# Performance work log

Hardware: AMD Instinct MI355X
Metric: run time of the kernel (lower is better)

The kernel has to match this reference:

```python
import jax, jax.numpy as jnp
import numpy as np

N = 100000
E = 1600000
D_IN = 128
H = 128


def _param(key, shape, scale=0.05):
    return jax.random.normal(key, shape, dtype=jnp.float32) * scale


def setup_inputs() -> dict:
    key = jax.random.key(0)
    ks = jax.random.split(key, 24)
    inp = {
        'x': jax.random.normal(ks[0], (N, D_IN), dtype=jnp.float32),
        'edge_index': jax.random.randint(ks[1], (2, E), 0, N, dtype=jnp.int64),
        'h1': jax.random.normal(ks[2], (N, H), dtype=jnp.float32),
        'h2': jax.random.normal(ks[3], (N, H), dtype=jnp.float32),
        'h3': jax.random.normal(ks[4], (N, H), dtype=jnp.float32),
        # GCNConv params (PyG: lin weight applied as x @ W, W: [in, out] here)
        'gcn1_w': _param(ks[5], (D_IN, H)),
        'gcn1_b': jnp.zeros((H,), jnp.float32),
        'gcn2_w': _param(ks[6], (H, H)),
        'gcn2_b': jnp.zeros((H,), jnp.float32),
    }
    # torch.nn.GRUCell params: weight_ih [3H, in], weight_hh [3H, H], biases [3H]
    for i, kw in zip((1, 2, 3), (ks[7], ks[10], ks[13])):
        k1, k2, k3 = jax.random.split(kw, 3)
        inp[f'gru{i}_wih'] = _param(k1, (3 * H, H))
        inp[f'gru{i}_whh'] = _param(k2, (3 * H, H))
        inp[f'gru{i}_bih'] = _param(k3, (3 * H,))
        inp[f'gru{i}_bhh'] = jnp.zeros((3 * H,), jnp.float32)
    return inp


def gcn_conv(x, src, dst, w, b):
    """PyG GCNConv: D^-1/2 (A+I) D^-1/2 X W + b (symmetric norm, self-loops)."""
    xw = x @ w  # [N, H]
    ones = jnp.ones((src.shape[0],), xw.dtype)
    # degree including self-loop
    deg = jax.ops.segment_sum(ones, dst, num_segments=N) + 1.0
    dinv = jax.lax.rsqrt(deg)
    norm = dinv[src] * dinv[dst]  # [E]
    agg = jax.ops.segment_sum(xw[src] * norm[:, None], dst, num_segments=N)
    # self-loop contribution: norm = dinv[i]*dinv[i] = 1/deg[i]
    return agg + xw / deg[:, None] + b


def gru_cell(x, h, w_ih, w_hh, b_ih, b_hh):
    gi = x @ w_ih.T + b_ih  # [N, 3H]
    gh = h @ w_hh.T + b_hh
    i_r, i_z, i_n = jnp.split(gi, 3, axis=-1)
    h_r, h_z, h_n = jnp.split(gh, 3, axis=-1)
    r = jax.nn.sigmoid(i_r + h_r)
    z = jax.nn.sigmoid(i_z + h_z)
    n = jnp.tanh(i_n + r * h_n)
    return (1.0 - z) * n + z * h


def reference(x, edge_index, h1, h2, h3,
              gcn1_w, gcn1_b, gcn2_w, gcn2_b,
              gru1_wih, gru1_whh, gru1_bih, gru1_bhh,
              gru2_wih, gru2_whh, gru2_bih, gru2_bhh,
              gru3_wih, gru3_whh, gru3_bih, gru3_bhh):
    src, dst = edge_index[0], edge_index[1]
    x = jax.nn.relu(gcn_conv(x, src, dst, gcn1_w, gcn1_b))
    # dropout is identity at eval
    x = jax.nn.relu(gcn_conv(x, src, dst, gcn2_w, gcn2_b))
    h1n = gru_cell(x, h1, gru1_wih, gru1_whh, gru1_bih, gru1_bhh)
    h2n = gru_cell(h1n, h2, gru2_wih, gru2_whh, gru2_bih, gru2_bhh)
    h3n = gru_cell(h2n, h3, gru3_wih, gru3_whh, gru3_bih, gru3_bhh)
    return (h1n, h2n, h3n)
```

## Files before the change

### kernel.cpp

```cpp
#include <hip/hip_runtime.h>
#include <hip/hip_bf16.h>

#define DH 128
#define SCB 1024
#define NCHUNK 256
#define LROW 136

typedef __attribute__((ext_vector_type(8))) short short8_t;
typedef __attribute__((ext_vector_type(4))) float f32x4;
typedef __attribute__((ext_vector_type(2))) float f32x2;

static __device__ __forceinline__ short f2bf(float f) {
    union { float f; unsigned u; } v; v.f = f;
    unsigned r = v.u + 0x7fffu + ((v.u >> 16) & 1u);
    return (short)(r >> 16);
}

static __device__ __forceinline__ float bf2f(unsigned short b) {
    union { unsigned u; float f; } v; v.u = ((unsigned)b) << 16;
    return v.f;
}

static __device__ __forceinline__ short8_t cvt8(const float* p) {
    float4 a0 = *(const float4*)p;
    float4 a1 = *(const float4*)(p + 4);
    short8_t t;
    t[0] = f2bf(a0.x); t[1] = f2bf(a0.y); t[2] = f2bf(a0.z); t[3] = f2bf(a0.w);
    t[4] = f2bf(a1.x); t[5] = f2bf(a1.y); t[6] = f2bf(a1.z); t[7] = f2bf(a1.w);
    return t;
}

static __device__ __forceinline__ short8_t cvt8v(float4 a0, float4 a1) {
    short8_t t;
    t[0] = f2bf(a0.x); t[1] = f2bf(a0.y); t[2] = f2bf(a0.z); t[3] = f2bf(a0.w);
    t[4] = f2bf(a1.x); t[5] = f2bf(a1.y); t[6] = f2bf(a1.z); t[7] = f2bf(a1.w);
    return t;
}

static __device__ __forceinline__ float sigm(float x) {
    return __builtin_amdgcn_rcpf(1.f + __expf(-x));
}
static __device__ __forceinline__ float tanh_f(float x) {
    return 1.f - 2.f * __builtin_amdgcn_rcpf(__expf(2.f * x) + 1.f);
}

__global__ __launch_bounds__(256) void deg2_k(const int* __restrict__ ei, int E,
                                              unsigned* __restrict__ cnt, int span, int chunkE) {
    int r = blockIdx.x & 7;
    int c = blockIdx.x >> 3;
    int lo = r * span, hi = lo + span;
    long long e0 = (long long)c * chunkE;
    long long e1 = e0 + chunkE; if (e1 > E) e1 = E;
    for (long long e = e0 + threadIdx.x; e < e1; e += 256) {
        int d = ei[E + e];
        if (d >= lo && d < hi) atomicAdd(&cnt[d], 1u);
    }
}

__global__ __launch_bounds__(256) void scan1_k(const unsigned* __restrict__ cnt, int N,
                                               int* __restrict__ offs, unsigned* __restrict__ bsum) {
    __shared__ unsigned s[256];
    int t = threadIdx.x;
    int i0 = blockIdx.x * SCB + t * 4;
    unsigned v0 = (i0 + 0 < N) ? cnt[i0 + 0] : 0u;
    unsigned v1 = (i0 + 1 < N) ? cnt[i0 + 1] : 0u;
    unsigned v2 = (i0 + 2 < N) ? cnt[i0 + 2] : 0u;
    unsigned v3 = (i0 + 3 < N) ? cnt[i0 + 3] : 0u;
    unsigned ts = v0 + v1 + v2 + v3;
    s[t] = ts;
    __syncthreads();
    for (int off = 1; off < 256; off <<= 1) {
        unsigned u = (t >= off) ? s[t - off] : 0u;
        __syncthreads();
        s[t] += u;
        __syncthreads();
    }
    unsigned ex = s[t] - ts;
    if (i0 + 0 < N) offs[i0 + 0] = (int)ex;
    if (i0 + 1 < N) offs[i0 + 1] = (int)(ex + v0);
    if (i0 + 2 < N) offs[i0 + 2] = (int)(ex + v0 + v1);
    if (i0 + 3 < N) offs[i0 + 3] = (int)(ex + v0 + v1 + v2);
    if (t == 255) bsum[blockIdx.x] = s[255];
}

__global__ __launch_bounds__(1024) void scan2_k(unsigned* __restrict__ bsum, int B) {
    __shared__ unsigned s[1024];
    int t = threadIdx.x;
    unsigned v = (t < B) ? bsum[t] : 0u;
    s[t] = v;
    __syncthreads();
    for (int off = 1; off < 1024; off <<= 1) {
        unsigned u = (t >= off) ? s[t - off] : 0u;
        __syncthreads();
        s[t] += u;
        __syncthreads();
    }
    if (t < B) bsum[t] = s[t] - v;
    if (t == 0) bsum[B] = s[1023];
}

__global__ void scan3_k(int* __restrict__ offs, int* __restrict__ cur,
                        float* __restrict__ dinv, const unsigned* __restrict__ cnt,
                        const unsigned* __restrict__ bsum, int N, int B) {
    int i = blockIdx.x * 256 + threadIdx.x;
    if (i < N) {
        int v = offs[i] + (int)bsum[i >> 10];
        offs[i] = v;
        cur[i] = v;
        dinv[i] = rsqrtf((float)cnt[i] + 1.0f);
    }
    if (i == 0) offs[N] = (int)bsum[B];
}

__global__ __launch_bounds__(256) void fill2_k(const int* __restrict__ ei, int E,
                                               int* __restrict__ cur, int* __restrict__ csr_src,
                                               int span, int chunkE) {
    int r = blockIdx.x & 7;
    int c = blockIdx.x >> 3;
    int lo = r * span, hi = lo + span;
    long long e0 = (long long)c * chunkE;
    long long e1 = e0 + chunkE; if (e1 > E) e1 = E;
    for (long long e = e0 + threadIdx.x; e < e1; e += 256) {
        int d = ei[E + e];
        if (d >= lo && d < hi) {
            int pos = atomicAdd(&cur[d], 1);
            csr_src[pos] = ei[e];
        }
    }
}

__global__ void f2bf6_k(const float* __restrict__ s0, const float* __restrict__ s1,
                        const float* __restrict__ s2, const float* __restrict__ s3,
                        const float* __restrict__ s4, const float* __restrict__ s5,
                        short* __restrict__ dst, int WN) {
    int i = blockIdx.x * 256 + threadIdx.x;
    if (i >= 6 * WN) return;
    int b = i / WN, r = i - b * WN;
    const float* srcs[6] = {s0, s1, s2, s3, s4, s5};
    dst[i] = f2bf(srcs[b][r]);
}

__global__ void transpose_bf2_k(const float* __restrict__ sa, const float* __restrict__ sb,
                                short* __restrict__ da, short* __restrict__ db) {
    int i = blockIdx.x * 256 + threadIdx.x;
    int m = i >> 14;
    int j = i & 16383;
    int c = j >> 7, k = j & 127;
    const float* s = m ? sb : sa;
    short* d = m ? db : da;
    d[j] = f2bf(s[k * DH + c]);
}

__global__ __launch_bounds__(256, 4) void gemm_mfma_k(const float* __restrict__ A,
                                                      const short* __restrict__ Wt,
                                                      const float* __restrict__ dinv,
                                                      unsigned char* __restrict__ C, int N) {
    int tid = threadIdx.x;
    int wave = tid >> 6, lane = tid & 63;
    int lr = lane & 15, kg = lane >> 4;

    int row0 = blockIdx.x * 128 + wave * 32;
    int ar0 = min(row0 + lr, N - 1);
    int ar1 = min(row0 + 16 + lr, N - 1);
    const float* a0p = A + (size_t)ar0 * DH;
    const float* a1p = A + (size_t)ar1 * DH;
    short8_t af[2][4];
#pragma unroll
    for (int ks = 0; ks < 4; ks++) {
        af[0][ks] = cvt8(a0p + ks * 32 + kg * 8);
        af[1][ks] = cvt8(a1p + ks * 32 + kg * 8);
    }

    float di0[4], di1[4];
#pragma unroll
    for (int j = 0; j < 4; j++) {
        di0[j] = dinv[min(row0 + kg * 4 + j, N - 1)];
        di1[j] = dinv[min(row0 + 16 + kg * 4 + j, N - 1)];
    }

    short8_t bt[3][4];
#define GLOADW(slot, t) { \
    const short* wp = Wt + (size_t)((t) * 16 + lr) * DH + kg * 8; \
    bt[slot][0] = *(const short8_t*)(wp); \
    bt[slot][1] = *(const short8_t*)(wp + 32); \
    bt[slot][2] = *(const short8_t*)(wp + 64); \
    bt[slot][3] = *(const short8_t*)(wp + 96); }

    GLOADW(0, 0)
    GLOADW(1, 1)
#pragma unroll
    for (int t = 0; t < 8; t++) {
        if (t < 6) GLOADW((t + 2) % 3, t + 2)
        f32x4 acc0 = {0.f, 0.f, 0.f, 0.f};
        f32x4 acc1 = {0.f, 0.f, 0.f, 0.f};
#pragma unroll
        for (int ks = 0; ks < 4; ks++) {
            acc0 = __builtin_amdgcn_mfma_f32_16x16x32_bf16(af[0][ks], bt[t % 3][ks], acc0, 0, 0, 0);
            acc1 = __builtin_amdgcn_mfma_f32_16x16x32_bf16(af[1][ks], bt[t % 3][ks], acc1, 0, 0, 0);
        }
        int col = t * 16 + lr;
#pragma unroll
        for (int j = 0; j < 4; j++) {
            int g0 = row0 + kg * 4 + j;
            int g1 = row0 + 16 + kg * 4 + j;
            float v0 = acc0[j] * di0[j];
            float v1 = acc1[j] * di1[j];
            if (g0 < N) C[(size_t)g0 * DH + col] =
                (unsigned char)__builtin_amdgcn_cvt_pk_fp8_f32(v0, v0, 0u, false);
            if (g1 < N) C[(size_t)g1 * DH + col] =
                (unsigned char)__builtin_amdgcn_cvt_pk_fp8_f32(v1, v1, 0u, false);
        }
    }
#undef GLOADW
}

__global__ __launch_bounds__(256) void gather_k(const int* __restrict__ csr_src,
                                                const int* __restrict__ offs,
                                                const float* __restrict__ dinv,
                                                const unsigned short* __restrict__ xq2,
                                                const float* __restrict__ bias,
                                                float* __restrict__ dest, int N) {
    int wid = blockIdx.x * 4 + (threadIdx.x >> 6);
    if (wid >= N) return;
    int lane = threadIdx.x & 63;
    int j = offs[wid];
    int end = offs[wid + 1];
    float dd = dinv[wid];

    f32x2 f0 = __builtin_amdgcn_cvt_pk_f32_fp8((unsigned)xq2[(size_t)wid * 64 + lane], false);
    float ax = f0[0];
    float ay = f0[1];

#define ACC(w) { f32x2 f_ = __builtin_amdgcn_cvt_pk_f32_fp8((unsigned)(w), false); \
                 ax += f_[0]; ay += f_[1]; }

    if (j + 4 <= end) {
        int a0 = csr_src[j], a1 = csr_src[j + 1], a2 = csr_src[j + 2], a3 = csr_src[j + 3];
        j += 4;
        for (; j + 4 <= end; j += 4) {
            unsigned w0 = xq2[(size_t)a0 * 64 + lane];
            unsigned w1 = xq2[(size_t)a1 * 64 + lane];
            unsigned w2 = xq2[(size_t)a2 * 64 + lane];
            unsigned w3 = xq2[(size_t)a3 * 64 + lane];
            a0 = csr_src[j]; a1 = csr_src[j + 1]; a2 = csr_src[j + 2]; a3 = csr_src[j + 3];
            ACC(w0) ACC(w1) ACC(w2) ACC(w3)
        }
        unsigned w0 = xq2[(size_t)a0 * 64 + lane];
        unsigned w1 = xq2[(size_t)a1 * 64 + lane];
        unsigned w2 = xq2[(size_t)a2 * 64 + lane];
        unsigned w3 = xq2[(size_t)a3 * 64 + lane];
        ACC(w0) ACC(w1) ACC(w2) ACC(w3)
    }
    for (; j < end; ++j) {
        unsigned w = xq2[(size_t)csr_src[j] * 64 + lane];
        ACC(w)
    }
#undef ACC

    float2 b2 = ((const float2*)bias)[lane];
    float ox = fmaxf(fmaf(dd, ax, b2.x), 0.f);
    float oy = fmaxf(fmaf(dd, ay, b2.y), 0.f);
    float2 o; o.x = ox; o.y = oy;
    ((float2*)dest)[(size_t)wid * 64 + lane] = o;
}

__global__ __launch_bounds__(512, 1) void gru3_mfma_k(
        const float* __restrict__ X, const float* __restrict__ H1,
        const float* __restrict__ H2, const float* __restrict__ H3,
        const short* __restrict__ w1i, const short* __restrict__ w1h,
        const short* __restrict__ w2i, const short* __restrict__ w2h,
        const short* __restrict__ w3i, const short* __restrict__ w3h,
        const float* __restrict__ bi1, const float* __restrict__ bh1,
        const float* __restrict__ bi2, const float* __restrict__ bh2,
        const float* __restrict__ bi3, const float* __restrict__ bh3,
        float* __restrict__ o1, float* __restrict__ o2, float* __restrict__ o3,
        int N) {
    __shared__ short lds[2][64 * LROW];
    int tid = threadIdx.x;
    int row0 = blockIdx.x * 64;
    int wave = tid >> 6, lane = tid & 63;
    int lr = lane & 15, kg = lane >> 4;
    int c0 = wave * 16;

    const short* wihs[3] = {w1i, w2i, w3i};
    const short* whhs[3] = {w1h, w2h, w3h};
    const float* bihs[3] = {bi1, bi2, bi3};
    const float* bhhs[3] = {bh1, bh2, bh3};
    float* outs[3] = {o1, o2, o3};

    short8_t bw[3][4], bu[3][4];
#define WLOADALL(wih_, whh_) { \
    _Pragma("unroll") \
    for (int g = 0; g < 3; g++) { \
        const short* wi = (wih_) + (size_t)(g * DH + c0 + lr) * DH + kg * 8; \
        const short* wh = (whh_) + (size_t)(g * DH + c0 + lr) * DH + kg * 8; \
        _Pragma("unroll") \
        for (int ks = 0; ks < 4; ks++) { \
            bw[g][ks] = *(const short8_t*)(wi + ks * 32); \
            bu[g][ks] = *(const short8_t*)(wh + ks * 32); \
        } \
    } }

    WLOADALL(w1i, w1h)

    {
        int mat = tid >> 8;
        int r = (tid & 255) >> 2;
        int q = tid & 3;
        int grow = min(row0 + r, N - 1);
        const float* src = (mat ? H1 : X) + (size_t)grow * DH + q * 32;
        char* dst = (char*)&lds[mat][r * LROW] + q * 64;
#pragma unroll
        for (int j = 0; j < 4; j++) {
            short8_t v = cvt8(src + j * 8);
            *(short8_t*)(dst + j * 16) = v;
        }
    }
    __syncthreads();

    int gcol = c0 + lr;
    int colb = gcol * 2;
    int srow = tid >> 3;
    int sq = tid & 7;

#pragma unroll
    for (int cell = 0; cell < 3; cell++) {
        f32x4 aR[4], aZ[4], aI[4], aH[4];
#pragma unroll
        for (int rt = 0; rt < 4; rt++) {
            aR[rt] = (f32x4){0,0,0,0}; aZ[rt] = (f32x4){0,0,0,0};
            aI[rt] = (f32x4){0,0,0,0}; aH[rt] = (f32x4){0,0,0,0};
        }
#pragma unroll
        for (int rt = 0; rt < 4; rt++) {
            int r = rt * 16 + lr;
            const char* xrow = (const char*)&lds[0][r * LROW];
            const char* hrow = (const char*)&lds[1][r * LROW];
            short8_t xa[4], ha[4];
#pragma unroll
            for (int ks = 0; ks < 4; ks++) {
                int boff = ks * 64 + kg * 16;
                xa[ks] = *(const short8_t*)(xrow + boff);
                ha[ks] = *(const short8_t*)(hrow + boff);
            }
#pragma unroll
            for (int ks = 0; ks < 4; ks++) {
                aR[rt] = __builtin_amdgcn_mfma_f32_16x16x32_bf16(xa[ks], bw[0][ks], aR[rt], 0, 0, 0);
                aR[rt] = __builtin_amdgcn_mfma_f32_16x16x32_bf16(ha[ks], bu[0][ks], aR[rt], 0, 0, 0);
                aZ[rt] = __builtin_amdgcn_mfma_f32_16x16x32_bf16(xa[ks], bw[1][ks], aZ[rt], 0, 0, 0);
                aZ[rt] = __builtin_amdgcn_mfma_f32_16x16x32_bf16(ha[ks], bu[1][ks], aZ[rt], 0, 0, 0);
                aI[rt] = __builtin_amdgcn_mfma_f32_16x16x32_bf16(xa[ks], bw[2][ks], aI[rt], 0, 0, 0);
                aH[rt] = __builtin_amdgcn_mfma_f32_16x16x32_bf16(ha[ks], bu[2][ks], aH[rt], 0, 0, 0);
            }
        }

        float4 hs0, hs1, hs2, hs3;
        if (cell < 2) {
            int grow = min(row0 + srow, N - 1);
            const float* src = (cell == 0 ? H2 : H3) + (size_t)grow * DH + sq * 16;
            hs0 = *(const float4*)(src + 0);
            hs1 = *(const float4*)(src + 4);
            hs2 = *(const float4*)(src + 8);
            hs3 = *(const float4*)(src + 12);
        }

        const float* bih = bihs[cell];
        const float* bhh = bhhs[cell];
        float br = bih[gcol], bz = bih[DH + gcol], bn = bih[2 * DH + gcol];
        float cr = bhh[gcol], cz = bhh[DH + gcol], cn = bhh[2 * DH + gcol];
        float* outp = outs[cell];
        short hb[4][4];
#pragma unroll
        for (int rt = 0; rt < 4; rt++) {
#pragma unroll
            for (int j = 0; j < 4; j++) {
                int r = rt * 16 + kg * 4 + j;
                float hv = bf2f(*(const unsigned short*)((const char*)&lds[1][r * LROW] + colb));
                float rr = sigm(aR[rt][j] + br + cr);
                float zz = sigm(aZ[rt][j] + bz + cz);
                float nn = tanh_f(aI[rt][j] + bn + rr * (aH[rt][j] + cn));
                float ov = (1.f - zz) * nn + zz * hv;
                int grow = row0 + r;
                if (grow < N) outp[(size_t)grow * DH + gcol] = ov;
                hb[rt][j] = f2bf(ov);
            }
        }

        if (cell < 2) {
            WLOADALL(wihs[cell + 1], whhs[cell + 1])
        }

        __syncthreads();

        if (cell < 2) {
#pragma unroll
            for (int rt = 0; rt < 4; rt++) {
#pragma unroll
                for (int j = 0; j < 4; j++) {
                    int r = rt * 16 + kg * 4 + j;
                    *(short*)((char*)&lds[0][r * LROW] + colb) = hb[rt][j];
                }
            }
            {
                char* dst = (char*)&lds[1][srow * LROW] + sq * 32;
                *(short8_t*)(dst) = cvt8v(hs0, hs1);
                *(short8_t*)(dst + 16) = cvt8v(hs2, hs3);
            }
            __syncthreads();
        }
    }
#undef WLOADALL
}

extern "C" void kernel_launch(void* const* d_in, const int* in_sizes, int n_in,
                              void* d_out, int out_size, void* d_ws, size_t ws_size,
                              hipStream_t stream) {
    const float* x    = (const float*)d_in[0];
    const int*   ei   = (const int*)d_in[1];
    const float* h1   = (const float*)d_in[2];
    const float* h2   = (const float*)d_in[3];
    const float* h3   = (const float*)d_in[4];
    const float* g1w  = (const float*)d_in[5];
    const float* g1b  = (const float*)d_in[6];
    const float* g2w  = (const float*)d_in[7];
    const float* g2b  = (const float*)d_in[8];
    const float* wih1 = (const float*)d_in[9];
    const float* whh1 = (const float*)d_in[10];
    const float* bih1 = (const float*)d_in[11];
    const float* bhh1 = (const float*)d_in[12];
    const float* wih2 = (const float*)d_in[13];
    const float* whh2 = (const float*)d_in[14];
    const float* bih2 = (const float*)d_in[15];
    const float* bhh2 = (const float*)d_in[16];
    const float* wih3 = (const float*)d_in[17];
    const float* whh3 = (const float*)d_in[18];
    const float* bih3 = (const float*)d_in[19];
    const float* bhh3 = (const float*)d_in[20];

    int N = in_sizes[0] / DH;
    int E = in_sizes[1] / 2;
    int B = (N + SCB - 1) / SCB;
    int nstripes = (N + 127) / 128;
    int nblk64 = (N + 63) / 64;
    int span = (N + 7) / 8;
    int chunkE = (E + NCHUNK - 1) / NCHUNK;

    char* wsp = (char*)d_ws;
    auto alloc = [&](size_t bytes) -> char* {
        char* p = wsp;
        wsp += (bytes + 63) & ~(size_t)63;
        return p;
    };
    unsigned* cnt = (unsigned*)alloc((size_t)N * 4);
    int* offs     = (int*)alloc(((size_t)N + 1) * 4);
    int* cur      = (int*)alloc((size_t)N * 4);
    float* dinv   = (float*)alloc((size_t)N * 4);
    unsigned* bsum= (unsigned*)alloc(((size_t)B + 1) * 4);
    int* csr_src  = (int*)alloc((size_t)E * 4);
    unsigned char* xq = (unsigned char*)alloc((size_t)N * DH);
    float* x2     = (float*)alloc((size_t)N * DH * 4);
    short* w1t    = (short*)alloc((size_t)DH * DH * 2);
    short* w2t    = (short*)alloc((size_t)DH * DH * 2);
    const int WN = 3 * DH * DH;
    short* wbAll  = (short*)alloc((size_t)6 * WN * 2);
    short* wb[6];
    for (int i = 0; i < 6; i++) wb[i] = wbAll + (size_t)i * WN;

    float* out  = (float*)d_out;
    float* h1n  = out;
    float* h2n  = out + (size_t)N * DH;
    float* h3n  = out + 2 * (size_t)N * DH;

    f2bf6_k<<<(6 * WN + 255) / 256, 256, 0, stream>>>(wih1, whh1, wih2, whh2, wih3, whh3, wbAll, WN);
    transpose_bf2_k<<<(2 * DH * DH + 255) / 256, 256, 0, stream>>>(g1w, g2w, w1t, w2t);

    hipMemsetAsync(cnt, 0, (size_t)N * 4, stream);
    deg2_k<<<8 * NCHUNK, 256, 0, stream>>>(ei, E, cnt, span, chunkE);
    scan1_k<<<B, 256, 0, stream>>>(cnt, N, offs, bsum);
    scan2_k<<<1, 1024, 0, stream>>>(bsum, B);
    scan3_k<<<(N + 255) / 256, 256, 0, stream>>>(offs, cur, dinv, cnt, bsum, N, B);
    fill2_k<<<8 * NCHUNK, 256, 0, stream>>>(ei, E, cur, csr_src, span, chunkE);

    int gblocks = (N + 3) / 4;

    gemm_mfma_k<<<nstripes, 256, 0, stream>>>(x, w1t, dinv, xq, N);
    gather_k<<<gblocks, 256, 0, stream>>>(csr_src, offs, dinv, (const unsigned short*)xq, g1b, x2, N);

    gemm_mfma_k<<<nstripes, 256, 0, stream>>>(x2, w2t, dinv, xq, N);
    gather_k<<<gblocks, 256, 0, stream>>>(csr_src, offs, dinv, (const unsigned short*)xq, g2b, x2, N);

    gru3_mfma_k<<<nblk64, 512, 0, stream>>>(x2, h1, h2, h3,
                                            wb[0], wb[1], wb[2], wb[3], wb[4], wb[5],
                                            bih1, bhh1, bih2, bhh2, bih3, bhh3,
                                            h1n, h2n, h3n, N);
}
```

Measured before the change: 531.0 us.

## Store intermediates in bf16 and make GRU kernel persistent with prefetch

The gather kernel now writes layer outputs as packed bf16 instead of fp32, and a new bf16-input GEMM consumes them directly, halving intermediate traffic. h1 is pre-converted to bf16 by a separate kernel. The GRU kernel becomes persistent over 512 blocks, with double-buffered LDS that prefetches the next stripe's X/H1 tiles during the last cell. The extra h1 conversion pass adds its own read and write of h1, and persistence may lower occupancy balance.

```diff
diff --git a/kernel.cpp b/kernel.cpp
--- a/kernel.cpp
+++ b/kernel.cpp
@@ -151,6 +151,14 @@
     d[j] = f2bf(s[k * DH + c]);
 }
 
+__global__ void h1bf_k(const float* __restrict__ src, unsigned* __restrict__ dst, long long n2) {
+    long long i = (long long)blockIdx.x * 256 + threadIdx.x;
+    if (i < n2) {
+        float2 v = ((const float2*)src)[i];
+        dst[i] = (unsigned)(unsigned short)f2bf(v.x) | ((unsigned)(unsigned short)f2bf(v.y) << 16);
+    }
+}
+
 __global__ __launch_bounds__(256, 4) void gemm_mfma_k(const float* __restrict__ A,
                                                       const short* __restrict__ Wt,
                                                       const float* __restrict__ dinv,
@@ -214,12 +222,75 @@
 #undef GLOADW
 }
 
+__global__ __launch_bounds__(256, 4) void gemm_mfma_bf_k(const short* __restrict__ A,
+                                                         const short* __restrict__ Wt,
+                                                         const float* __restrict__ dinv,
+                                                         unsigned char* __restrict__ C, int N) {
+    int tid = threadIdx.x;
+    int wave = tid >> 6, lane = tid & 63;
+    int lr = lane & 15, kg = lane >> 4;
+
+    int row0 = blockIdx.x * 128 + wave * 32;
+    int ar0 = min(row0 + lr, N - 1);
+    int ar1 = min(row0 + 16 + lr, N - 1);
+    const short* a0p = A + (size_t)ar0 * DH;
+    const short* a1p = A + (size_t)ar1 * DH;
+    short8_t af[2][4];
+#pragma unroll
+    for (int ks = 0; ks < 4; ks++) {
+        af[0][ks] = *(const short8_t*)(a0p + ks * 32 + kg * 8);
+        af[1][ks] = *(const short8_t*)(a1p + ks * 32 + kg * 8);
+    }
+
+    float di0[4], di1[4];
+#pragma unroll
+    for (int j = 0; j < 4; j++) {
+        di0[j] = dinv[min(row0 + kg * 4 + j, N - 1)];
+        di1[j] = dinv[min(row0 + 16 + kg * 4 + j, N - 1)];
+    }
+
+    short8_t bt[3][4];
+#define GLOADW(slot, t) { \
+    const short* wp = Wt + (size_t)((t) * 16 + lr) * DH + kg * 8; \
+    bt[slot][0] = *(const short8_t*)(wp); \
+    bt[slot][1] = *(const short8_t*)(wp + 32); \
+    bt[slot][2] = *(const short8_t*)(wp + 64); \
+    bt[slot][3] = *(const short8_t*)(wp + 96); }
+
+    GLOADW(0, 0)
+    GLOADW(1, 1)
+#pragma unroll
+    for (int t = 0; t < 8; t++) {
+        if (t < 6) GLOADW((t + 2) % 3, t + 2)
+        f32x4 acc0 = {0.f, 0.f, 0.f, 0.f};
+        f32x4 acc1 = {0.f, 0.f, 0.f, 0.f};
+#pragma unroll
+        for (int ks = 0; ks < 4; ks++) {
+            acc0 = __builtin_amdgcn_mfma_f32_16x16x32_bf16(af[0][ks], bt[t % 3][ks], acc0, 0, 0, 0);
+            acc1 = __builtin_amdgcn_mfma_f32_16x16x32_bf16(af[1][ks], bt[t % 3][ks], acc1, 0, 0, 0);
+        }
+        int col = t * 16 + lr;
+#pragma unroll
+        for (int j = 0; j < 4; j++) {
+            int g0 = row0 + kg * 4 + j;
+            int g1 = row0 + 16 + kg * 4 + j;
+            float v0 = acc0[j] * di0[j];
+            float v1 = acc1[j] * di1[j];
+            if (g0 < N) C[(size_t)g0 * DH + col] =
+                (unsigned char)__builtin_amdgcn_cvt_pk_fp8_f32(v0, v0, 0u, false);
+            if (g1 < N) C[(size_t)g1 * DH + col] =
+                (unsigned char)__builtin_amdgcn_cvt_pk_fp8_f32(v1, v1, 0u, false);
+        }
+    }
+#undef GLOADW
+}
+
 __global__ __launch_bounds__(256) void gather_k(const int* __restrict__ csr_src,
                                                 const int* __restrict__ offs,
                                                 const float* __restrict__ dinv,
                                                 const unsigned short* __restrict__ xq2,
                                                 const float* __restrict__ bias,
-                                                float* __restrict__ dest, int N) {
+                                                unsigned* __restrict__ dest, int N) {
     int wid = blockIdx.x * 4 + (threadIdx.x >> 6);
     if (wid >= N) return;
     int lane = threadIdx.x & 63;
@@ -260,12 +331,13 @@
     float2 b2 = ((const float2*)bias)[lane];
     float ox = fmaxf(fmaf(dd, ax, b2.x), 0.f);
     float oy = fmaxf(fmaf(dd, ay, b2.y), 0.f);
-    float2 o; o.x = ox; o.y = oy;
-    ((float2*)dest)[(size_t)wid * 64 + lane] = o;
-}
-
-__global__ __launch_bounds__(512, 1) void gru3_mfma_k(
-        const float* __restrict__ X, const float* __restrict__ H1,
+    unsigned o = (unsigned)(unsigned short)f2bf(ox) | ((unsigned)(unsigned short)f2bf(oy) << 16);
+    dest[(size_t)wid * 64 + lane] = o;
+}
+
+__global__ __launch_bounds__(512, 1) void gru3p_mfma_k(
+        const unsigned* __restrict__ Xb,
+        const unsigned* __restrict__ H1b,
         const float* __restrict__ H2, const float* __restrict__ H3,
         const short* __restrict__ w1i, const short* __restrict__ w1h,
         const short* __restrict__ w2i, const short* __restrict__ w2h,
@@ -274,10 +346,9 @@
         const float* __restrict__ bi2, const float* __restrict__ bh2,
         const float* __restrict__ bi3, const float* __restrict__ bh3,
         float* __restrict__ o1, float* __restrict__ o2, float* __restrict__ o3,
-        int N) {
-    __shared__ short lds[2][64 * LROW];
+        int N, int nstripes) {
+    __shared__ short lds[2][2][64 * LROW];
     int tid = threadIdx.x;
-    int row0 = blockIdx.x * 64;
     int wave = tid >> 6, lane = tid & 63;
     int lr = lane & 15, kg = lane >> 4;
     int c0 = wave * 16;
@@ -303,111 +374,140 @@
 
     WLOADALL(w1i, w1h)
 
-    {
-        int mat = tid >> 8;
-        int r = (tid & 255) >> 2;
-        int q = tid & 3;
-        int grow = min(row0 + r, N - 1);
-        const float* src = (mat ? H1 : X) + (size_t)grow * DH + q * 32;
-        char* dst = (char*)&lds[mat][r * LROW] + q * 64;
-#pragma unroll
-        for (int j = 0; j < 4; j++) {
-            short8_t v = cvt8(src + j * 8);
-            *(short8_t*)(dst + j * 16) = v;
-        }
-    }
-    __syncthreads();
-
     int gcol = c0 + lr;
     int colb = gcol * 2;
     int srow = tid >> 3;
     int sq = tid & 7;
-
-#pragma unroll
-    for (int cell = 0; cell < 3; cell++) {
-        f32x4 aR[4], aZ[4], aI[4], aH[4];
-#pragma unroll
-        for (int rt = 0; rt < 4; rt++) {
-            aR[rt] = (f32x4){0,0,0,0}; aZ[rt] = (f32x4){0,0,0,0};
-            aI[rt] = (f32x4){0,0,0,0}; aH[rt] = (f32x4){0,0,0,0};
-        }
-#pragma unroll
-        for (int rt = 0; rt < 4; rt++) {
-            int r = rt * 16 + lr;
-            const char* xrow = (const char*)&lds[0][r * LROW];
-            const char* hrow = (const char*)&lds[1][r * LROW];
-            short8_t xa[4], ha[4];
-#pragma unroll
-            for (int ks = 0; ks < 4; ks++) {
-                int boff = ks * 64 + kg * 16;
-                xa[ks] = *(const short8_t*)(xrow + boff);
-                ha[ks] = *(const short8_t*)(hrow + boff);
+    int pmat = tid >> 8;
+    int prow = (tid & 255) >> 2;
+    int pq = tid & 3;
+
+    int s = blockIdx.x;
+    if (s >= nstripes) return;
+
+    {
+        int grow = min(s * 64 + prow, N - 1);
+        const uint4* src4 = (const uint4*)((pmat ? H1b : Xb) + (size_t)grow * 64 + pq * 16);
+        uint4 a = src4[0], b = src4[1], c = src4[2], d = src4[3];
+        char* dst = (char*)&lds[0][pmat][prow * LROW] + pq * 64;
+        *(uint4*)(dst + 0)  = a;
+        *(uint4*)(dst + 16) = b;
+        *(uint4*)(dst + 32) = c;
+        *(uint4*)(dst + 48) = d;
+    }
+    __syncthreads();
+
+    int cur = 0;
+    for (; s < nstripes; ) {
+        int row0 = s * 64;
+        int snext = s + gridDim.x;
+        bool hasnext = snext < nstripes;
+        short* ldsX = lds[cur][0];
+        short* ldsH = lds[cur][1];
+        short* nxtX = lds[cur ^ 1][0];
+        short* nxtH = lds[cur ^ 1][1];
+        uint4 px0, px1, px2, px3;
+
+#pragma unroll
+        for (int cell = 0; cell < 3; cell++) {
+            f32x4 aR[4], aZ[4], aI[4], aH[4];
+#pragma unroll
+            for (int rt = 0; rt < 4; rt++) {
+                aR[rt] = (f32x4){0,0,0,0}; aZ[rt] = (f32x4){0,0,0,0};
+                aI[rt] = (f32x4){0,0,0,0}; aH[rt] = (f32x4){0,0,0,0};
             }
 #pragma unroll
-            for (int ks = 0; ks < 4; ks++) {
-                aR[rt] = __builtin_amdgcn_mfma_f32_16x16x32_bf16(xa[ks], bw[0][ks], aR[rt], 0, 0, 0);
-                aR[rt] = __builtin_amdgcn_mfma_f32_16x16x32_bf16(ha[ks], bu[0][ks], aR[rt], 0, 0, 0);
-                aZ[rt] = __builtin_amdgcn_mfma_f32_16x16x32_bf16(xa[ks], bw[1][ks], aZ[rt], 0, 0, 0);
-                aZ[rt] = __builtin_amdgcn_mfma_f32_16x16x32_bf16(ha[ks], bu[1][ks], aZ[rt], 0, 0, 0);
-                aI[rt] = __builtin_amdgcn_mfma_f32_16x16x32_bf16(xa[ks], bw[2][ks], aI[rt], 0, 0, 0);
-                aH[rt] = __builtin_amdgcn_mfma_f32_16x16x32_bf16(ha[ks], bu[2][ks], aH[rt], 0, 0, 0);
+            for (int rt = 0; rt < 4; rt++) {
+                int r = rt * 16 + lr;
+                const char* xrow = (const char*)&ldsX[r * LROW];
+                const char* hrow = (const char*)&ldsH[r * LROW];
+                short8_t xa[4], ha[4];
+#pragma unroll
+                for (int ks = 0; ks < 4; ks++) {
+                    int boff = ks * 64 + kg * 16;
+                    xa[ks] = *(const short8_t*)(xrow + boff);
+                    ha[ks] = *(const short8_t*)(hrow + boff);
+                }
+#pragma unroll
+                for (int ks = 0; ks < 4; ks++) {
+                    aR[rt] = __builtin_amdgcn_mfma_f32_16x16x32_bf16(xa[ks], bw[0][ks], aR[rt], 0, 0, 0);
+                    aR[rt] = __builtin_amdgcn_mfma_f32_16x16x32_bf16(ha[ks], bu[0][ks], aR[rt], 0, 0, 0);
+                    aZ[rt] = __builtin_amdgcn_mfma_f32_16x16x32_bf16(xa[ks], bw[1][ks], aZ[rt], 0, 0, 0);
+                    aZ[rt] = __builtin_amdgcn_mfma_f32_16x16x32_bf16(ha[ks], bu[1][ks], aZ[rt], 0, 0, 0);
+                    aI[rt] = __builtin_amdgcn_mfma_f32_16x16x32_bf16(xa[ks], bw[2][ks], aI[rt], 0, 0, 0);
+                    aH[rt] = __builtin_amdgcn_mfma_f32_16x16x32_bf16(ha[ks], bu[2][ks], aH[rt], 0, 0, 0);
+                }
             }
-        }
-
-        float4 hs0, hs1, hs2, hs3;
-        if (cell < 2) {
-            int grow = min(row0 + srow, N - 1);
-            const float* src = (cell == 0 ? H2 : H3) + (size_t)grow * DH + sq * 16;
-            hs0 = *(const float4*)(src + 0);
-            hs1 = *(const float4*)(src + 4);
-            hs2 = *(const float4*)(src + 8);
-            hs3 = *(const float4*)(src + 12);
-        }
-
-        const float* bih = bihs[cell];
-        const float* bhh = bhhs[cell];
-        float br = bih[gcol], bz = bih[DH + gcol], bn = bih[2 * DH + gcol];
-        float cr = bhh[gcol], cz = bhh[DH + gcol], cn = bhh[2 * DH + gcol];
-        float* outp = outs[cell];
-        short hb[4][4];
-#pragma unroll
-        for (int rt = 0; rt < 4; rt++) {
-#pragma unroll
-            for (int j = 0; j < 4; j++) {
-                int r = rt * 16 + kg * 4 + j;
-                float hv = bf2f(*(const unsigned short*)((const char*)&lds[1][r * LROW] + colb));
-                float rr = sigm(aR[rt][j] + br + cr);
-                float zz = sigm(aZ[rt][j] + bz + cz);
-                float nn = tanh_f(aI[rt][j] + bn + rr * (aH[rt][j] + cn));
-                float ov = (1.f - zz) * nn + zz * hv;
-                int grow = row0 + r;
-                if (grow < N) outp[(size_t)grow * DH + gcol] = ov;
-                hb[rt][j] = f2bf(ov);
+
+            float4 hs0, hs1, hs2, hs3;
+            if (cell < 2) {
+                int grow = min(row0 + srow, N - 1);
+                const float* src = (cell == 0 ? H2 : H3) + (size_t)grow * DH + sq * 16;
+                hs0 = *(const float4*)(src + 0);
+                hs1 = *(const float4*)(src + 4);
+                hs2 = *(const float4*)(src + 8);
+                hs3 = *(const float4*)(src + 12);
+            } else if (hasnext) {
+                int grow = min(snext * 64 + prow, N - 1);
+                const uint4* src4 = (const uint4*)((pmat ? H1b : Xb) + (size_t)grow * 64 + pq * 16);
+                px0 = src4[0]; px1 = src4[1]; px2 = src4[2]; px3 = src4[3];
             }
-        }
-
-        if (cell < 2) {
-            WLOADALL(wihs[cell + 1], whhs[cell + 1])
-        }
-
-        __syncthreads();
-
-        if (cell < 2) {
+
+            const float* bih = bihs[cell];
+            const float* bhh = bhhs[cell];
+            float br = bih[gcol], bz = bih[DH + gcol], bn = bih[2 * DH + gcol];
+            float cr = bhh[gcol], cz = bhh[DH + gcol], cn = bhh[2 * DH + gcol];
+            float* outp = outs[cell];
+            short hb[4][4];
 #pragma unroll
             for (int rt = 0; rt < 4; rt++) {
 #pragma unroll
                 for (int j = 0; j < 4; j++) {
                     int r = rt * 16 + kg * 4 + j;
-                    *(short*)((char*)&lds[0][r * LROW] + colb) = hb[rt][j];
+                    float hv = bf2f(*(const unsigned short*)((const char*)&ldsH[r * LROW] + colb));
+                    float rr = sigm(aR[rt][j] + br + cr);
+                    float zz = sigm(aZ[rt][j] + bz + cz);
+                    float nn = tanh_f(aI[rt][j] + bn + rr * (aH[rt][j] + cn));
+                    float ov = (1.f - zz) * nn + zz * hv;
+                    int grow = row0 + r;
+                    if (grow < N) outp[(size_t)grow * DH + gcol] = ov;
+                    hb[rt][j] = f2bf(ov);
                 }
             }
-            {
-                char* dst = (char*)&lds[1][srow * LROW] + sq * 32;
-                *(short8_t*)(dst) = cvt8v(hs0, hs1);
-                *(short8_t*)(dst + 16) = cvt8v(hs2, hs3);
+
+            if (cell < 2) {
+                WLOADALL(wihs[cell + 1], whhs[cell + 1])
+            } else if (hasnext) {
+                WLOADALL(w1i, w1h)
             }
-            __syncthreads();
-        }
+
+            if (cell < 2) {
+                __syncthreads();
+#pragma unroll
+                for (int rt = 0; rt < 4; rt++) {
+#pragma unroll
+                    for (int j = 0; j < 4; j++) {
+                        int r = rt * 16 + kg * 4 + j;
+                        *(short*)((char*)&ldsX[r * LROW] + colb) = hb[rt][j];
+                    }
+                }
+                {
+                    char* dst = (char*)&ldsH[srow * LROW] + sq * 32;
+                    *(short8_t*)(dst) = cvt8v(hs0, hs1);
+                    *(short8_t*)(dst + 16) = cvt8v(hs2, hs3);
+                }
+                __syncthreads();
+            } else if (hasnext) {
+                char* dst = (char*)&(pmat ? nxtH : nxtX)[prow * LROW] + pq * 64;
+                *(uint4*)(dst + 0)  = px0;
+                *(uint4*)(dst + 16) = px1;
+                *(uint4*)(dst + 32) = px2;
+                *(uint4*)(dst + 48) = px3;
+                __syncthreads();
+            }
+        }
+        cur ^= 1;
+        s = snext;
     }
 #undef WLOADALL
 }
@@ -458,7 +558,8 @@
     unsigned* bsum= (unsigned*)alloc(((size_t)B + 1) * 4);
     int* csr_src  = (int*)alloc((size_t)E * 4);
     unsigned char* xq = (unsigned char*)alloc((size_t)N * DH);
-    float* x2     = (float*)alloc((size_t)N * DH * 4);
+    unsigned* x2b = (unsigned*)alloc((size_t)N * DH * 2);
+    unsigned* h1b = (unsigned*)alloc((size_t)N * DH * 2);
     short* w1t    = (short*)alloc((size_t)DH * DH * 2);
     short* w2t    = (short*)alloc((size_t)DH * DH * 2);
     const int WN = 3 * DH * DH;
@@ -473,6 +574,8 @@
 
     f2bf6_k<<<(6 * WN + 255) / 256, 256, 0, stream>>>(wih1, whh1, wih2, whh2, wih3, whh3, wbAll, WN);
     transpose_bf2_k<<<(2 * DH * DH + 255) / 256, 256, 0, stream>>>(g1w, g2w, w1t, w2t);
+    long long n2 = (long long)N * DH / 2;
+    h1bf_k<<<(int)((n2 + 255) / 256), 256, 0, stream>>>(h1, h1b, n2);
 
     hipMemsetAsync(cnt, 0, (size_t)N * 4, stream);
     deg2_k<<<8 * NCHUNK, 256, 0, stream>>>(ei, E, cnt, span, chunkE);
@@ -484,13 +587,13 @@
     int gblocks = (N + 3) / 4;
 
     gemm_mfma_k<<<nstripes, 256, 0, stream>>>(x, w1t, dinv, xq, N);
-    gather_k<<<gblocks, 256, 0, stream>>>(csr_src, offs, dinv, (const unsigned short*)xq, g1b, x2, N);
-
-    gemm_mfma_k<<<nstripes, 256, 0, stream>>>(x2, w2t, dinv, xq, N);
-    gather_k<<<gblocks, 256, 0, stream>>>(csr_src, offs, dinv, (const unsigned short*)xq, g2b, x2, N);
-
-    gru3_mfma_k<<<nblk64, 512, 0, stream>>>(x2, h1, h2, h3,
-                                            wb[0], wb[1], wb[2], wb[3], wb[4], wb[5],
-                                            bih1, bhh1, bih2, bhh2, bih3, bhh3,
-                                            h1n, h2n, h3n, N);
-}
+    gather_k<<<gblocks, 256, 0, stream>>>(csr_src, offs, dinv, (const unsigned short*)xq, g1b, x2b, N);
+
+    gemm_mfma_bf_k<<<nstripes, 256, 0, stream>>>((const short*)x2b, w2t, dinv, xq, N);
+    gather_k<<<gblocks, 256, 0, stream>>>(csr_src, offs, dinv, (const unsigned short*)xq, g2b, x2b, N);
+
+    gru3p_mfma_k<<<512, 512, 0, stream>>>(x2b, h1b, h2, h3,
+                                          wb[0], wb[1], wb[2], wb[3], wb[4], wb[5],
+                                          bih1, bhh1, bih2, bhh2, bih3, bhh3,
+                                          h1n, h2n, h3n, N, nblk64);
+}
```

New measurement: 686.6 us. 1.29x slower.
